# Kernel optimization log

Hardware: AMD Instinct MI355X
Metric: run time of the kernel (lower is better)

## Reference

```python
import jax, jax.numpy as jnp
import numpy as np

B, IN, S, PD, P, D = 8192, 19000, 256, 128, 16, 64  # batch, input_dim, shared_dim, pathway_dim, n_pathways, n_drugs


def setup_inputs() -> dict:
    key = jax.random.key(0)
    ks = jax.random.split(key, 6)
    x = jax.random.normal(ks[0], (B, IN), dtype=jnp.float32)
    drug_indices = jax.random.randint(ks[1], (B,), 0, D, dtype=jnp.int32)
    W1 = jax.random.normal(ks[2], (IN, S), dtype=jnp.float32) / np.float32(np.sqrt(IN))
    b1 = jnp.zeros((S,), jnp.float32)
    Wp = jax.random.normal(ks[3], (P, S, PD), dtype=jnp.float32) / np.float32(np.sqrt(S))
    bp = jnp.zeros((P, PD), jnp.float32)
    Wd = jax.random.normal(ks[4], (D, PD), dtype=jnp.float32) / np.float32(np.sqrt(PD))
    bd = jnp.zeros((D,), jnp.float32)
    drug_to_pw = (jnp.arange(D, dtype=jnp.int32) % P)  # drug -> pathway routing table (i%16 per init_kwargs)
    return dict(x=x, drug_indices=drug_indices, W1=W1, b1=b1, Wp=Wp, bp=bp, Wd=Wd, bd=bd, drug_to_pw=drug_to_pw)


def reference(x, drug_indices, W1, b1, Wp, bp, Wd, bd, drug_to_pw):
    # shared encoder (dropout is identity in eval)
    h = jax.nn.relu(x @ W1 + b1)                                  # [B, S]
    # run all pathway experts densely (P is small), then per-sample select
    all_pw = jax.nn.relu(jnp.einsum('bs,psd->bpd', h, Wp) + bp)   # [B, P, PD]
    pw_idx = drug_to_pw[drug_indices]                             # [B]
    pw_out = jnp.take_along_axis(all_pw, pw_idx[:, None, None], axis=1)[:, 0]  # [B, PD]
    # per-sample drug head: gather row of Wd and dot
    out = jnp.sum(pw_out * Wd[drug_indices], axis=-1) + bd[drug_indices]       # [B]
    return out
```

## Files before the change

kernel.cpp:

```cpp
#include <hip/hip_runtime.h>

#define KREAL 19000
#define KP    19008
#define NSTEPS 594
#define BM 128
#define BN 256
#define MBLK 64
#define BATCH 8192
#define SDIM 256
#define PDIM 128

typedef __attribute__((ext_vector_type(8))) short frag_ab;
typedef __attribute__((ext_vector_type(4))) float frag_cd;

static __device__ __forceinline__ short f2bf(float f) {
    union { float f; unsigned u; } cv; cv.f = f;
    unsigned u = cv.u;
    u += 0x7fffu + ((u >> 16) & 1u);
    return (short)(u >> 16);
}

__global__ void transpose_w1(const float* __restrict__ W1, short* __restrict__ W1t) {
    __shared__ float tile[32][33];
    int k0 = blockIdx.x * 32;
    int n0 = blockIdx.y * 32;
    int tx = threadIdx.x & 31;
    int ty = threadIdx.x >> 5;
#pragma unroll
    for (int i = 0; i < 32; i += 8) {
        int k = k0 + ty + i;
        tile[ty + i][tx] = (k < KREAL) ? W1[(long)k * SDIM + n0 + tx] : 0.f;
    }
    __syncthreads();
#pragma unroll
    for (int i = 0; i < 32; i += 8) {
        int n = n0 + ty + i;
        W1t[(long)n * KP + k0 + tx] = f2bf(tile[tx][ty + i]);
    }
}

__global__ __launch_bounds__(512, 2)
void gemm1(const float* __restrict__ x, const short* __restrict__ W1t,
           float* __restrict__ pout, int nch) {
    __shared__ short As[BM * 32];
    __shared__ short Bs[BN * 32];

    int mb = blockIdx.x;
    int ch = blockIdx.y;
    int m0 = mb * BM;
    int s0 = (NSTEPS * ch) / nch;
    int s1 = (NSTEPS * (ch + 1)) / nch;

    int tid  = threadIdx.x;
    int wave = tid >> 6;
    int lane = tid & 63;
    int wr = wave >> 2, wc = wave & 3;
    int lrow = lane & 15;
    int lq   = lane >> 4;

    frag_cd acc[4][4];
#pragma unroll
    for (int i = 0; i < 4; i++)
#pragma unroll
        for (int j = 0; j < 4; j++) acc[i][j] = (frag_cd)(0.f);

    for (int s = s0; s < s1; s++) {
        int kb = s * 32;
#pragma unroll
        for (int r = 0; r < 2; r++) {
            int idx = tid + 512 * r;
            int row = idx >> 3;
            int k4  = (idx & 7) * 4;
            int gk  = kb + k4;
            float4 v;
            if (gk + 4 <= KREAL) {
                v = *(const float4*)(x + (long)(m0 + row) * KREAL + gk);
            } else {
                v = make_float4(0.f, 0.f, 0.f, 0.f);
            }
            short4 p;
            p.x = f2bf(v.x); p.y = f2bf(v.y); p.z = f2bf(v.z); p.w = f2bf(v.w);
            *(short4*)(&As[row * 32 + k4]) = p;
        }
#pragma unroll
        for (int r = 0; r < 2; r++) {
            int idx  = tid + 512 * r;
            int n    = idx >> 2;
            int koff = (idx & 3) * 8;
            int4 v = *(const int4*)(W1t + (long)n * KP + kb + koff);
            *(int4*)(&Bs[n * 32 + koff]) = v;
        }
        __syncthreads();

        frag_ab af[4], bf[4];
#pragma unroll
        for (int mt = 0; mt < 4; mt++)
            af[mt] = *(const frag_ab*)(&As[(wr * 64 + mt * 16 + lrow) * 32 + lq * 8]);
#pragma unroll
        for (int nt = 0; nt < 4; nt++)
            bf[nt] = *(const frag_ab*)(&Bs[(wc * 64 + nt * 16 + lrow) * 32 + lq * 8]);
#pragma unroll
        for (int mt = 0; mt < 4; mt++)
#pragma unroll
            for (int nt = 0; nt < 4; nt++)
                acc[mt][nt] = __builtin_amdgcn_mfma_f32_16x16x32_bf16(
                    af[mt], bf[nt], acc[mt][nt], 0, 0, 0);
        __syncthreads();
    }

#pragma unroll
    for (int mt = 0; mt < 4; mt++)
#pragma unroll
        for (int nt = 0; nt < 4; nt++)
#pragma unroll
            for (int r = 0; r < 4; r++) {
                int row = m0 + wr * 64 + mt * 16 + lq * 4 + r;
                int col = wc * 64 + nt * 16 + lrow;
                pout[((long)ch * BATCH + row) * SDIM + col] = acc[mt][nt][r];
            }
}

__global__ void stage2(const float* __restrict__ pout, const float* __restrict__ b1,
                       const float* __restrict__ Wp, const float* __restrict__ bp,
                       const float* __restrict__ Wd, const float* __restrict__ bd,
                       const int* __restrict__ drug_idx, const int* __restrict__ d2p,
                       float* __restrict__ out, int nch) {
    __shared__ float h[SDIM];
    __shared__ float red[2];
    int b = blockIdx.x;
    int t = threadIdx.x;
    int drug = drug_idx[b];
    int p    = d2p[drug];

    for (int i = t; i < SDIM; i += 128) {
        float a = b1[i];
        for (int c = 0; c < nch; c++)
            a += pout[((long)c * BATCH + b) * SDIM + i];
        h[i] = fmaxf(a, 0.f);
    }
    __syncthreads();

    const float* wp = Wp + (long)p * SDIM * PDIM;
    float a = 0.f;
#pragma unroll 8
    for (int s = 0; s < SDIM; s++)
        a = fmaf(h[s], wp[s * PDIM + t], a);
    a += bp[p * PDIM + t];
    a = fmaxf(a, 0.f);

    float v = a * Wd[drug * PDIM + t];
#pragma unroll
    for (int off = 32; off; off >>= 1) v += __shfl_down(v, off, 64);
    if ((t & 63) == 0) red[t >> 6] = v;
    __syncthreads();
    if (t == 0) out[b] = red[0] + red[1] + bd[drug];
}

extern "C" void kernel_launch(void* const* d_in, const int* in_sizes, int n_in,
                              void* d_out, int out_size, void* d_ws, size_t ws_size,
                              hipStream_t stream) {
    const float* x    = (const float*)d_in[0];
    const int*   drug = (const int*)d_in[1];
    const float* W1   = (const float*)d_in[2];
    const float* b1   = (const float*)d_in[3];
    const float* Wp   = (const float*)d_in[4];
    const float* bp   = (const float*)d_in[5];
    const float* Wd   = (const float*)d_in[6];
    const float* bd   = (const float*)d_in[7];
    const int*   d2p  = (const int*)d_in[8];
    float* out = (float*)d_out;

    size_t pchunk    = (size_t)BATCH * SDIM * sizeof(float);
    size_t w1t_bytes = (size_t)SDIM * KP * sizeof(short);
    int nch = 4;
    if (ws_size < w1t_bytes + 4 * pchunk) {
        long avail = (long)ws_size - (long)w1t_bytes;
        nch = (int)(avail / (long)pchunk);
        if (nch < 1) nch = 1;
        if (nch > 4) nch = 4;
    }
    float* pout = (float*)d_ws;
    short* W1t  = (short*)((char*)d_ws + (size_t)nch * pchunk);

    hipLaunchKernelGGL(transpose_w1, dim3(NSTEPS, SDIM / 32), dim3(256), 0, stream,
                       W1, W1t);
    hipLaunchKernelGGL(gemm1, dim3(MBLK, nch), dim3(512), 0, stream,
                       x, W1t, pout, nch);
    hipLaunchKernelGGL(stage2, dim3(BATCH), dim3(128), 0, stream,
                       pout, b1, Wp, bp, Wd, bd, drug, d2p, out, nch);
}
```

Before: 951.3 us.

## Double-buffer LDS with register prefetch and XCD-aware block mapping in gemm1

The main GEMM now stages the next K-step's global loads into registers while the current step runs its MFMAs. It ping-pongs between two LDS buffers, which drops one barrier per iteration. The grid is flattened and block ids are remapped so that blocks sharing a K-chunk of W1t land on the same XCD, improving L2 reuse. This costs twice the LDS and more registers, which could reduce occupancy under the 512-thread, 2-block launch bounds.

```diff
diff --git a/kernel.cpp b/kernel.cpp
--- a/kernel.cpp
+++ b/kernel.cpp
@@ -20,6 +20,12 @@
     return (short)(u >> 16);
 }
 
+static __device__ __forceinline__ short4 cvt4(float4 v) {
+    short4 p;
+    p.x = f2bf(v.x); p.y = f2bf(v.y); p.z = f2bf(v.z); p.w = f2bf(v.w);
+    return p;
+}
+
 __global__ void transpose_w1(const float* __restrict__ W1, short* __restrict__ W1t) {
     __shared__ float tile[32][33];
     int k0 = blockIdx.x * 32;
@@ -42,11 +48,20 @@
 __global__ __launch_bounds__(512, 2)
 void gemm1(const float* __restrict__ x, const short* __restrict__ W1t,
            float* __restrict__ pout, int nch) {
-    __shared__ short As[BM * 32];
-    __shared__ short Bs[BN * 32];
-
-    int mb = blockIdx.x;
-    int ch = blockIdx.y;
+    __shared__ short As[2][BM * 32];
+    __shared__ short Bs[2][BN * 32];
+
+    int bid = blockIdx.x;
+    int mb, ch;
+    if (nch == 4) {
+        int xcd  = bid & 7;
+        int slot = bid >> 3;
+        ch = xcd >> 1;
+        mb = ((xcd & 1) << 5) | slot;
+    } else {
+        mb = bid % MBLK;
+        ch = bid / MBLK;
+    }
     int m0 = mb * BM;
     int s0 = (NSTEPS * ch) / nch;
     int s1 = (NSTEPS * (ch + 1)) / nch;
@@ -58,54 +73,58 @@
     int lrow = lane & 15;
     int lq   = lane >> 4;
 
+    int k4 = (tid & 7) << 2;
+    const float* xp0 = x + (long)(m0 + (tid >> 3)) * KREAL + k4;
+    const float* xp1 = xp0 + (long)64 * KREAL;
+    const short* bp0 = W1t + (long)(tid >> 2) * KP + ((tid & 3) << 3);
+    const short* bp1 = bp0 + (long)128 * KP;
+
     frag_cd acc[4][4];
 #pragma unroll
     for (int i = 0; i < 4; i++)
 #pragma unroll
         for (int j = 0; j < 4; j++) acc[i][j] = (frag_cd)(0.f);
 
-    for (int s = s0; s < s1; s++) {
-        int kb = s * 32;
-#pragma unroll
-        for (int r = 0; r < 2; r++) {
-            int idx = tid + 512 * r;
-            int row = idx >> 3;
-            int k4  = (idx & 7) * 4;
-            int gk  = kb + k4;
-            float4 v;
-            if (gk + 4 <= KREAL) {
-                v = *(const float4*)(x + (long)(m0 + row) * KREAL + gk);
-            } else {
-                v = make_float4(0.f, 0.f, 0.f, 0.f);
-            }
-            short4 p;
-            p.x = f2bf(v.x); p.y = f2bf(v.y); p.z = f2bf(v.z); p.w = f2bf(v.w);
-            *(short4*)(&As[row * 32 + k4]) = p;
-        }
-#pragma unroll
-        for (int r = 0; r < 2; r++) {
-            int idx  = tid + 512 * r;
-            int n    = idx >> 2;
-            int koff = (idx & 3) * 8;
-            int4 v = *(const int4*)(W1t + (long)n * KP + kb + koff);
-            *(int4*)(&Bs[n * 32 + koff]) = v;
+    float4 ra0, ra1;
+    int4   rb0, rb1;
+    {
+        int kb = s0 * 32;
+        bool ok = (kb + k4 + 4 <= KREAL);
+        ra0 = ok ? *(const float4*)(xp0 + kb) : make_float4(0.f, 0.f, 0.f, 0.f);
+        ra1 = ok ? *(const float4*)(xp1 + kb) : make_float4(0.f, 0.f, 0.f, 0.f);
+        rb0 = *(const int4*)(bp0 + kb);
+        rb1 = *(const int4*)(bp1 + kb);
+    }
+
+    int buf = 0;
+    for (int s = s0; s < s1; ++s) {
+        *(short4*)(&As[buf][tid * 4])        = cvt4(ra0);
+        *(short4*)(&As[buf][tid * 4 + 2048]) = cvt4(ra1);
+        *(int4*)(&Bs[buf][tid * 8])          = rb0;
+        *(int4*)(&Bs[buf][tid * 8 + 4096])   = rb1;
+        if (s + 1 < s1) {
+            int kb = (s + 1) * 32;
+            bool ok = (kb + k4 + 4 <= KREAL);
+            ra0 = ok ? *(const float4*)(xp0 + kb) : make_float4(0.f, 0.f, 0.f, 0.f);
+            ra1 = ok ? *(const float4*)(xp1 + kb) : make_float4(0.f, 0.f, 0.f, 0.f);
+            rb0 = *(const int4*)(bp0 + kb);
+            rb1 = *(const int4*)(bp1 + kb);
         }
         __syncthreads();
-
-        frag_ab af[4], bf[4];
+        frag_ab af[4], bfr[4];
 #pragma unroll
         for (int mt = 0; mt < 4; mt++)
-            af[mt] = *(const frag_ab*)(&As[(wr * 64 + mt * 16 + lrow) * 32 + lq * 8]);
+            af[mt] = *(const frag_ab*)(&As[buf][(wr * 64 + mt * 16 + lrow) * 32 + lq * 8]);
 #pragma unroll
         for (int nt = 0; nt < 4; nt++)
-            bf[nt] = *(const frag_ab*)(&Bs[(wc * 64 + nt * 16 + lrow) * 32 + lq * 8]);
+            bfr[nt] = *(const frag_ab*)(&Bs[buf][(wc * 64 + nt * 16 + lrow) * 32 + lq * 8]);
 #pragma unroll
         for (int mt = 0; mt < 4; mt++)
 #pragma unroll
             for (int nt = 0; nt < 4; nt++)
                 acc[mt][nt] = __builtin_amdgcn_mfma_f32_16x16x32_bf16(
-                    af[mt], bf[nt], acc[mt][nt], 0, 0, 0);
-        __syncthreads();
+                    af[mt], bfr[nt], acc[mt][nt], 0, 0, 0);
+        buf ^= 1;
     }
 
 #pragma unroll
@@ -184,7 +203,7 @@
 
     hipLaunchKernelGGL(transpose_w1, dim3(NSTEPS, SDIM / 32), dim3(256), 0, stream,
                        W1, W1t);
-    hipLaunchKernelGGL(gemm1, dim3(MBLK, nch), dim3(512), 0, stream,
+    hipLaunchKernelGGL(gemm1, dim3(MBLK * nch), dim3(512), 0, stream,
                        x, W1t, pout, nch);
     hipLaunchKernelGGL(stage2, dim3(BATCH), dim3(128), 0, stream,
                        pout, b1, Wp, bp, Wd, bd, drug, d2p, out, nch);
```

Result: faster. 910.4 us (-4.3%).
